# Kernel optimization log

Measured on AMD Instinct MI355X. Metric: run time of the kernel, lower is better.

## Reference

```python
import jax, jax.numpy as jnp
import numpy as np

HEADS = 16
DIM_HEAD = 64
SCALE = DIM_HEAD ** -0.5


def setup_inputs() -> dict:
    key = jax.random.key(0)
    k1, k2, k3, k4 = jax.random.split(key, 4)
    b, n, dim = 2, 2048, 1024
    inner = HEADS * DIM_HEAD  # 1024
    x = jax.random.normal(k1, (b, n, dim), dtype=jnp.float32)
    mask = jax.random.randint(k2, (b, n), 0, 2, dtype=jnp.int32)
    Wqkv = jax.random.normal(k3, (dim, inner), dtype=jnp.float32) * (dim ** -0.5)
    Wout = jax.random.normal(k4, (inner, dim), dtype=jnp.float32) * (inner ** -0.5)
    bout = jnp.zeros((dim,), dtype=jnp.float32)
    return {"x": x, "mask": mask, "Wqkv": Wqkv, "Wout": Wout, "bout": bout}


def reference(x, mask, Wqkv, Wout, bout):
    b, n, _ = x.shape
    # shared projection: w acts as q = k = v (CRATE subspace attention)
    w = jnp.einsum('bnd,de->bne', x, Wqkv)
    w = w.reshape(b, n, HEADS, DIM_HEAD).transpose(0, 2, 1, 3)  # b h n d
    dots = jnp.einsum('bhid,bhjd->bhij', w, w) * SCALE           # b h n n
    attn = jax.nn.softmax(dots, axis=-1)
    # post-softmax multiplicative masking (mask=1 zeros the column)
    m = mask[:, None, None, :].astype(attn.dtype)
    attn = attn * (1.0 - m)
    out = jnp.einsum('bhij,bhjd->bhid', attn, w)                 # b h n d
    out = out.transpose(0, 2, 1, 3).reshape(b, n, HEADS * DIM_HEAD)
    return jnp.einsum('bne,ed->bnd', out, Wout) + bout
```

## Files before the change

kernel.cpp:

```cpp
#include <hip/hip_runtime.h>
#include <hip/hip_bf16.h>
#include <stdint.h>

typedef unsigned short u16;
typedef unsigned int u32;
typedef __bf16 bf16x8 __attribute__((ext_vector_type(8)));
typedef float f32x4 __attribute__((ext_vector_type(4)));
typedef float f32x16 __attribute__((ext_vector_type(16)));
typedef u32 u32x4 __attribute__((ext_vector_type(4)));

#define AS1 __attribute__((address_space(1)))
#define AS3 __attribute__((address_space(3)))

__device__ __forceinline__ void async16(const u16* g, u16* l) {
  __builtin_amdgcn_global_load_lds((const AS1 uint32_t*)(const void*)g,
                                   (AS3 uint32_t*)l, 16, 0, 0);
}

__device__ __forceinline__ u16 f2bf(float v) {
  union { __hip_bfloat16 b; u16 u; } c; c.b = __float2bfloat16(v); return c.u;
}

__device__ __forceinline__ u32 pkbf(float a, float b) {
  u32 r;
  asm("v_cvt_pk_bf16_f32 %0, %1, %2" : "=v"(r) : "v"(a), "v"(b));
  return r;
}

__device__ __forceinline__ void swap32(u32 &a, u32 &b) {
  asm("v_permlane32_swap_b32 %0, %1" : "+v"(a), "+v"(b));
}

#if __has_builtin(__builtin_amdgcn_exp2f)
#define fast_exp2(x) __builtin_amdgcn_exp2f(x)
#else
#define fast_exp2(x) exp2f(x)
#endif

#if __has_builtin(__builtin_amdgcn_rcpf)
#define fast_rcp(x) __builtin_amdgcn_rcpf(x)
#else
#define fast_rcp(x) (1.0f / (x))
#endif

__device__ __forceinline__ uint4 pack8(float4 lo, float4 hi) {
  uint4 q;
  q.x = (u32)f2bf(lo.x) | ((u32)f2bf(lo.y) << 16);
  q.y = (u32)f2bf(lo.z) | ((u32)f2bf(lo.w) << 16);
  q.z = (u32)f2bf(hi.x) | ((u32)f2bf(hi.y) << 16);
  q.w = (u32)f2bf(hi.z) | ((u32)f2bf(hi.w) << 16);
  return q;
}

__global__ void cvt_x(const float* __restrict__ in, u16* __restrict__ out) {
  int i = (blockIdx.x * 256 + threadIdx.x) * 8;
  float4 lo = *(const float4*)(in + i);
  float4 hi = *(const float4*)(in + i + 4);
  *(uint4*)(out + i) = pack8(lo, hi);
}

__global__ void transpose1024_cvt2(const float* __restrict__ in0, u16* __restrict__ out0,
                                   const float* __restrict__ in1, u16* __restrict__ out1) {
  const float* in = blockIdx.z ? in1 : in0;
  u16* out = blockIdx.z ? out1 : out0;
  __shared__ u16 tile[32][33];
  int tx = threadIdx.x, ty = threadIdx.y;
  int c0 = blockIdx.x * 32, r0 = blockIdx.y * 32;
#pragma unroll
  for (int i = 0; i < 32; i += 8)
    tile[ty + i][tx] = f2bf(in[(size_t)(r0 + ty + i) * 1024 + c0 + tx]);
  __syncthreads();
#pragma unroll
  for (int i = 0; i < 32; i += 8)
    out[(size_t)(c0 + ty + i) * 1024 + r0 + tx] = tile[tx][ty + i];
}

__global__ void scale_transpose_v(const u16* __restrict__ w, const int* __restrict__ mask,
                                  u16* __restrict__ Vt) {
  __shared__ u16 tile[32][33];
  const int tx = threadIdx.x, ty = threadIdx.y;
  const int j0 = blockIdx.x * 32, d0 = blockIdx.y * 32;
  const int bh = blockIdx.z, b = bh >> 4, hc = (bh & 15) * 64;
#pragma unroll
  for (int i = 0; i < 32; i += 8) {
    int j = j0 + ty + i;
    u16 v = w[(size_t)(b * 2048 + j) * 1024 + hc + d0 + tx];
    tile[ty + i][tx] = mask[b * 2048 + j] ? (u16)0 : v;
  }
  __syncthreads();
#pragma unroll
  for (int i = 0; i < 32; i += 8)
    Vt[((size_t)bh * 64 + d0 + ty + i) * 2048 + j0 + tx] = tile[tx][ty + i];
}

template<bool OUT_F32>
__launch_bounds__(256)
__global__ void gemm_bt(const u16* __restrict__ A, const u16* __restrict__ BT,
                        void* __restrict__ Cp, const float* __restrict__ bias,
                        int M, int N, int K) {
  __shared__ __align__(16) u16 As[2][128 * 64];
  __shared__ __align__(16) u16 Bs[2][64 * 64];
  const int t = threadIdx.x;
  const int lane = t & 63, wave = t >> 6;
  const int wgid = blockIdx.x + gridDim.x * blockIdx.y;
  const int chunk = wgid & 7, ii = wgid >> 3;
  const int m0 = ((chunk & 3) * 8 + (ii & 7)) * 128;
  const int n0 = ((chunk >> 2) * 8 + (ii >> 3)) * 64;
  const int wm = (wave & 1) * 64, wn = (wave >> 1) * 32;
  const int lrow = lane & 15, quad = lane >> 4;

  f32x4 acc[4][2] = {};

  const int ar = t >> 2, ac = (t & 3) * 8;
  const u16* gA = A + (size_t)(m0 + ar) * K + ac;
  const u16* gB = BT + (size_t)(n0 + ar) * K + ac;

#define GSTAGE(buf, k0s) do { \
    async16(gA + (k0s),                       &As[buf][t * 8]); \
    async16(gA + (k0s) + (size_t)64 * K,      &As[buf][t * 8 + 2048]); \
    async16(gA + (k0s) + 32,                  &As[buf][4096 + t * 8]); \
    async16(gA + (k0s) + 32 + (size_t)64 * K, &As[buf][4096 + t * 8 + 2048]); \
    async16(gB + (k0s),                       &Bs[buf][t * 8]); \
    async16(gB + (k0s) + 32,                  &Bs[buf][2048 + t * 8]); \
  } while (0)

  GSTAGE(0, 0);

  int cur = 0;
  for (int k0 = 0; k0 < K; k0 += 64) {
    if (k0 + 64 < K) {
      GSTAGE(cur ^ 1, k0 + 64);
      asm volatile("s_waitcnt vmcnt(6)" ::: "memory");
    } else {
      asm volatile("s_waitcnt vmcnt(0)" ::: "memory");
    }
    __builtin_amdgcn_s_barrier();
    __builtin_amdgcn_sched_barrier(0);

#pragma unroll
    for (int kk = 0; kk < 2; kk++) {
      bf16x8 af[4], bfr[2];
#pragma unroll
      for (int i = 0; i < 4; i++)
        af[i] = *(const bf16x8*)&As[cur][kk * 4096 + (wm + i * 16 + lrow) * 32 + quad * 8];
#pragma unroll
      for (int j = 0; j < 2; j++)
        bfr[j] = *(const bf16x8*)&Bs[cur][kk * 2048 + (wn + j * 16 + lrow) * 32 + quad * 8];
#pragma unroll
      for (int i = 0; i < 4; i++)
#pragma unroll
        for (int j = 0; j < 2; j++)
          acc[i][j] = __builtin_amdgcn_mfma_f32_16x16x32_bf16(af[i], bfr[j], acc[i][j], 0, 0, 0);
    }
    asm volatile("s_waitcnt lgkmcnt(0)" ::: "memory");
    __builtin_amdgcn_sched_barrier(0);
    __builtin_amdgcn_s_barrier();
    __builtin_amdgcn_sched_barrier(0);
    cur ^= 1;
  }
#undef GSTAGE

  float bv[2];
#pragma unroll
  for (int j = 0; j < 2; j++)
    bv[j] = bias ? bias[n0 + wn + j * 16 + lrow] : 0.f;

#pragma unroll
  for (int i = 0; i < 4; i++) {
#pragma unroll
    for (int r = 0; r < 4; r++) {
      int row = m0 + wm + i * 16 + quad * 4 + r;
#pragma unroll
      for (int j = 0; j < 2; j++) {
        size_t ci = (size_t)row * N + n0 + wn + j * 16 + lrow;
        float v = acc[i][j][r] + bv[j];
        if (OUT_F32) ((float*)Cp)[ci] = v;
        else ((u16*)Cp)[ci] = f2bf(v);
      }
    }
  }
}

#define C1 0.18033688f
#define C2 -28.853901f
__launch_bounds__(512)
__global__ void attn_kernel(const u16* __restrict__ w, const u16* __restrict__ Vt,
                            u16* __restrict__ y) {
  __shared__ __align__(16) u16 smem[2][2][2][64 * 64];
  const int t = threadIdx.x, lane = t & 63, wv = t >> 6;
  const int qg = wv & 3, kgr = wv >> 2;
  const int ql = lane & 31, hi = lane >> 5, swz = ql & 7;
  const int wgid = blockIdx.x + 16 * blockIdx.y;
  const int newid = (wgid & 7) * 64 + (wgid >> 3);
  const int bh = newid >> 4, b = bh >> 4, hc = (bh & 15) * 64;
  const int q0 = (newid & 15) * 128;
  const size_t rowb = (size_t)b * 2048;

  const int tt = t & 255;
  const int sg = t >> 8;
  const int skey = tt >> 3;
  const int scl = ((tt & 7) ^ (skey & 7)) * 8;
  const int sjb = sg * 1024;
  const u16* kptr = w + rowb * 1024 + hc;
  const u16* vptr = Vt + (size_t)bh * 64 * 2048;

  bf16x8 qf[4];
  {
    const size_t qrow = rowb + q0 + qg * 32 + ql;
#pragma unroll
    for (int ks = 0; ks < 4; ks++)
      qf[ks] = *(const bf16x8*)&w[qrow * 1024 + hc + ks * 16 + hi * 8];
  }

  union { u32x4 u; bf16x8 bf; } ones;
  ones.u = (u32x4){0x3F803F80u, 0x3F803F80u, 0x3F803F80u, 0x3F803F80u};

  f32x16 o0 = {}, o1 = {};
  f32x16 den = {};

#define STAGE(buf, j0s) do { \
    async16(kptr + (size_t)(sjb + (j0s) + skey) * 1024 + scl,       &smem[0][sg][buf][tt * 8]); \
    async16(kptr + (size_t)(sjb + (j0s) + skey + 32) * 1024 + scl,  &smem[0][sg][buf][2048 + tt * 8]); \
    async16(vptr + (size_t)skey * 2048 + sjb + (j0s) + scl,         &smem[1][sg][buf][tt * 8]); \
    async16(vptr + (size_t)(skey + 32) * 2048 + sjb + (j0s) + scl,  &smem[1][sg][buf][2048 + tt * 8]); \
  } while (0)

  STAGE(0, 0);
  __syncthreads();

  int cur = 0;
  for (int j0 = 0; j0 < 1024; j0 += 64) {
    if (j0 + 64 < 1024) STAGE(cur ^ 1, j0 + 64);

    const u16* Wt = smem[0][kgr][cur];
    const u16* Vts = smem[1][kgr][cur];

    u32x4 pa[4];
#pragma unroll
    for (int g = 0; g < 2; g++) {
      f32x16 p = {};
#pragma unroll
      for (int ks = 0; ks < 4; ks++) {
        bf16x8 af = *(const bf16x8*)
            &Wt[(g * 32 + ql) * 64 + (((ks * 2 + hi) ^ swz) * 8)];
        p = __builtin_amdgcn_mfma_f32_32x32x16_bf16(af, qf[ks], p, 0, 0, 0);
      }
      float e[16];
#pragma unroll
      for (int r = 0; r < 16; r++)
        e[r] = fast_exp2(fmaf(p[r], C1, C2));
      u32 a0 = pkbf(e[0], e[1]),   b0 = pkbf(e[4], e[5]);   swap32(a0, b0);
      u32 a1 = pkbf(e[2], e[3]),   b1 = pkbf(e[6], e[7]);   swap32(a1, b1);
      u32 a2 = pkbf(e[8], e[9]),   b2 = pkbf(e[12], e[13]); swap32(a2, b2);
      u32 a3 = pkbf(e[10], e[11]), b3 = pkbf(e[14], e[15]); swap32(a3, b3);
      u32x4 f0 = {a0, a1, b0, b1};
      u32x4 f1 = {a2, a3, b2, b3};
      pa[2 * g + 0] = f0;
      pa[2 * g + 1] = f1;
    }

    __builtin_amdgcn_s_setprio(1);
#pragma unroll
    for (int ks = 0; ks < 4; ks++) {
      union { u32x4 u; bf16x8 bf; } cv; cv.u = pa[ks];
      bf16x8 vb0 = *(const bf16x8*)
          &Vts[ql * 64 + (((ks * 2 + hi) ^ swz) * 8)];
      bf16x8 vb1 = *(const bf16x8*)
          &Vts[(32 + ql) * 64 + (((ks * 2 + hi) ^ swz) * 8)];
      o0 = __builtin_amdgcn_mfma_f32_32x32x16_bf16(cv.bf, vb0, o0, 0, 0, 0);
      o1 = __builtin_amdgcn_mfma_f32_32x32x16_bf16(cv.bf, vb1, o1, 0, 0, 0);
      den = __builtin_amdgcn_mfma_f32_32x32x16_bf16(cv.bf, ones.bf, den, 0, 0, 0);
    }
    __builtin_amdgcn_s_setprio(0);

    __syncthreads();
    cur ^= 1;
  }
#undef STAGE

  float* mrg = (float*)smem;
  float* slot = mrg + (qg * 64 + lane) * 49;
  if (kgr == 1) {
#pragma unroll
    for (int r = 0; r < 16; r++) {
      slot[r] = o0[r]; slot[16 + r] = o1[r]; slot[32 + r] = den[r];
    }
  }
  __syncthreads();
  if (kgr == 0) {
#pragma unroll
    for (int r = 0; r < 16; r++) {
      o0[r] += slot[r]; o1[r] += slot[16 + r]; den[r] += slot[32 + r];
    }
#pragma unroll
    for (int r = 0; r < 16; r++) {
      const int qo = (r & 3) + 8 * (r >> 2) + 4 * hi;
      const float iv = fast_rcp(den[r]);
      const size_t orow = rowb + q0 + qg * 32 + qo;
      y[orow * 1024 + hc + ql]      = f2bf(o0[r] * iv);
      y[orow * 1024 + hc + 32 + ql] = f2bf(o1[r] * iv);
    }
  }
}

extern "C" void kernel_launch(void* const* d_in, const int* in_sizes, int n_in,
                              void* d_out, int out_size, void* d_ws, size_t ws_size,
                              hipStream_t stream) {
  const float* x    = (const float*)d_in[0];
  const int* mask   = (const int*)d_in[1];
  const float* Wqkv = (const float*)d_in[2];
  const float* Wout = (const float*)d_in[3];
  const float* bout = (const float*)d_in[4];
  float* out = (float*)d_out;

  u16* w     = (u16*)d_ws;
  u16* y     = w + 4096 * 1024;
  u16* WqkvT = y + 4096 * 1024;
  u16* WoutT = WqkvT + 1024 * 1024;
  u16* Vt    = WoutT + 1024 * 1024;
  u16* xb    = y;

  cvt_x<<<2048, 256, 0, stream>>>(x, xb);
  transpose1024_cvt2<<<dim3(32, 32, 2), dim3(32, 8), 0, stream>>>(Wqkv, WqkvT, Wout, WoutT);
  gemm_bt<false><<<dim3(32, 16), 256, 0, stream>>>(xb, WqkvT, w, nullptr, 4096, 1024, 1024);
  scale_transpose_v<<<dim3(64, 2, 32), dim3(32, 8), 0, stream>>>(w, mask, Vt);
  attn_kernel<<<dim3(16, 32), 512, 0, stream>>>(w, Vt, y);
  gemm_bt<true><<<dim3(32, 16), 256, 0, stream>>>(y, WoutT, out, bout, 4096, 1024, 1024);
}
```

Before: 163.1 us.

## Retile projection GEMMs to 64x64 tiles with 32x32 MFMA and swizzled LDS

The projection GEMM now uses 64x64 output tiles per block instead of 128x64, which doubles the grid to 1024 blocks so more CUs are occupied. Each wave computes a 32x32 sub-tile with the 32x32x16 bf16 MFMA. The LDS layout moves to full 64-element rows with an XOR swizzle to avoid bank conflicts. Smaller tiles mean less operand reuse per block and more global traffic, in exchange for better parallelism and fewer LDS reads per MFMA.

```diff
diff --git a/kernel.cpp b/kernel.cpp
--- a/kernel.cpp
+++ b/kernel.cpp
@@ -98,30 +98,29 @@
 __global__ void gemm_bt(const u16* __restrict__ A, const u16* __restrict__ BT,
                         void* __restrict__ Cp, const float* __restrict__ bias,
                         int M, int N, int K) {
-  __shared__ __align__(16) u16 As[2][128 * 64];
+  __shared__ __align__(16) u16 As[2][64 * 64];
   __shared__ __align__(16) u16 Bs[2][64 * 64];
   const int t = threadIdx.x;
   const int lane = t & 63, wave = t >> 6;
+  const int ql = lane & 31, hi = lane >> 5, swz = ql & 7;
   const int wgid = blockIdx.x + gridDim.x * blockIdx.y;
-  const int chunk = wgid & 7, ii = wgid >> 3;
-  const int m0 = ((chunk & 3) * 8 + (ii & 7)) * 128;
-  const int n0 = ((chunk >> 2) * 8 + (ii >> 3)) * 64;
-  const int wm = (wave & 1) * 64, wn = (wave >> 1) * 32;
-  const int lrow = lane & 15, quad = lane >> 4;
-
-  f32x4 acc[4][2] = {};
-
-  const int ar = t >> 2, ac = (t & 3) * 8;
-  const u16* gA = A + (size_t)(m0 + ar) * K + ac;
-  const u16* gB = BT + (size_t)(n0 + ar) * K + ac;
+  const int c = wgid & 7, ii = wgid >> 3;
+  const int m0 = (c * 8 + (ii & 7)) * 64;
+  const int n0 = (ii >> 3) * 64;
+  const int wm = (wave & 1) * 32, wn = (wave >> 1) * 32;
+
+  f32x16 acc = {};
+
+  const int sr = t >> 3;
+  const int sc8 = ((t & 7) ^ (sr & 7)) * 8;
+  const u16* gAt = A + (size_t)(m0 + sr) * K + sc8;
+  const u16* gBt = BT + (size_t)(n0 + sr) * K + sc8;
 
 #define GSTAGE(buf, k0s) do { \
-    async16(gA + (k0s),                       &As[buf][t * 8]); \
-    async16(gA + (k0s) + (size_t)64 * K,      &As[buf][t * 8 + 2048]); \
-    async16(gA + (k0s) + 32,                  &As[buf][4096 + t * 8]); \
-    async16(gA + (k0s) + 32 + (size_t)64 * K, &As[buf][4096 + t * 8 + 2048]); \
-    async16(gB + (k0s),                       &Bs[buf][t * 8]); \
-    async16(gB + (k0s) + 32,                  &Bs[buf][2048 + t * 8]); \
+    async16(gAt + (k0s),                   &As[buf][t * 8]); \
+    async16(gAt + (k0s) + (size_t)32 * K,  &As[buf][t * 8 + 2048]); \
+    async16(gBt + (k0s),                   &Bs[buf][t * 8]); \
+    async16(gBt + (k0s) + (size_t)32 * K,  &Bs[buf][t * 8 + 2048]); \
   } while (0)
 
   GSTAGE(0, 0);
@@ -130,7 +129,7 @@
   for (int k0 = 0; k0 < K; k0 += 64) {
     if (k0 + 64 < K) {
       GSTAGE(cur ^ 1, k0 + 64);
-      asm volatile("s_waitcnt vmcnt(6)" ::: "memory");
+      asm volatile("s_waitcnt vmcnt(4)" ::: "memory");
     } else {
       asm volatile("s_waitcnt vmcnt(0)" ::: "memory");
     }
@@ -138,19 +137,10 @@
     __builtin_amdgcn_sched_barrier(0);
 
 #pragma unroll
-    for (int kk = 0; kk < 2; kk++) {
-      bf16x8 af[4], bfr[2];
-#pragma unroll
-      for (int i = 0; i < 4; i++)
-        af[i] = *(const bf16x8*)&As[cur][kk * 4096 + (wm + i * 16 + lrow) * 32 + quad * 8];
-#pragma unroll
-      for (int j = 0; j < 2; j++)
-        bfr[j] = *(const bf16x8*)&Bs[cur][kk * 2048 + (wn + j * 16 + lrow) * 32 + quad * 8];
-#pragma unroll
-      for (int i = 0; i < 4; i++)
-#pragma unroll
-        for (int j = 0; j < 2; j++)
-          acc[i][j] = __builtin_amdgcn_mfma_f32_16x16x32_bf16(af[i], bfr[j], acc[i][j], 0, 0, 0);
+    for (int kk = 0; kk < 4; kk++) {
+      bf16x8 af = *(const bf16x8*)&As[cur][(wm + ql) * 64 + (((2 * kk + hi) ^ swz) * 8)];
+      bf16x8 bfr = *(const bf16x8*)&Bs[cur][(wn + ql) * 64 + (((2 * kk + hi) ^ swz) * 8)];
+      acc = __builtin_amdgcn_mfma_f32_32x32x16_bf16(af, bfr, acc, 0, 0, 0);
     }
     asm volatile("s_waitcnt lgkmcnt(0)" ::: "memory");
     __builtin_amdgcn_sched_barrier(0);
@@ -160,24 +150,16 @@
   }
 #undef GSTAGE
 
-  float bv[2];
-#pragma unroll
-  for (int j = 0; j < 2; j++)
-    bv[j] = bias ? bias[n0 + wn + j * 16 + lrow] : 0.f;
-
-#pragma unroll
-  for (int i = 0; i < 4; i++) {
-#pragma unroll
-    for (int r = 0; r < 4; r++) {
-      int row = m0 + wm + i * 16 + quad * 4 + r;
-#pragma unroll
-      for (int j = 0; j < 2; j++) {
-        size_t ci = (size_t)row * N + n0 + wn + j * 16 + lrow;
-        float v = acc[i][j][r] + bv[j];
-        if (OUT_F32) ((float*)Cp)[ci] = v;
-        else ((u16*)Cp)[ci] = f2bf(v);
-      }
-    }
+  const float bv = bias ? bias[n0 + wn + ql] : 0.f;
+  const int col = n0 + wn + ql;
+
+#pragma unroll
+  for (int r = 0; r < 16; r++) {
+    const int row = m0 + wm + (r & 3) + 8 * (r >> 2) + 4 * hi;
+    const size_t ci = (size_t)row * N + col;
+    const float v = acc[r] + bv;
+    if (OUT_F32) ((float*)Cp)[ci] = v;
+    else ((u16*)Cp)[ci] = f2bf(v);
   }
 }
 
@@ -322,8 +304,8 @@
 
   cvt_x<<<2048, 256, 0, stream>>>(x, xb);
   transpose1024_cvt2<<<dim3(32, 32, 2), dim3(32, 8), 0, stream>>>(Wqkv, WqkvT, Wout, WoutT);
-  gemm_bt<false><<<dim3(32, 16), 256, 0, stream>>>(xb, WqkvT, w, nullptr, 4096, 1024, 1024);
+  gemm_bt<false><<<dim3(64, 16), 256, 0, stream>>>(xb, WqkvT, w, nullptr, 4096, 1024, 1024);
   scale_transpose_v<<<dim3(64, 2, 32), dim3(32, 8), 0, stream>>>(w, mask, Vt);
   attn_kernel<<<dim3(16, 32), 512, 0, stream>>>(w, Vt, y);
-  gemm_bt<true><<<dim3(32, 16), 256, 0, stream>>>(y, WoutT, out, bout, 4096, 1024, 1024);
-}
+  gemm_bt<true><<<dim3(64, 16), 256, 0, stream>>>(y, WoutT, out, bout, 4096, 1024, 1024);
+}
```

After: 160.5 us. Within noise of the previous version (-1.6%).
